# Optimization experiments

Hardware: AMD Instinct MI355X
Metric: run time of the kernel (lower is better)

The kernel has to match this reference:

```python
import jax, jax.numpy as jnp
import numpy as np

F = 128          # feature_size
C = 300          # n_content_dims
V = 100001       # n_nodes + 1 (embedding rows)
N0, N1, N2 = 409600, 40960, 4096   # NodeFlow layer sizes (fanout ~10)
E0, E1 = 409600, 40960             # edges in block0 (L0->L1) and block1 (L1->L2)


def setup_inputs() -> dict:
    key = jax.random.key(0)
    ks = jax.random.split(key, 24)
    std = 1.0 / F
    xav_p = float(np.sqrt(6.0 / (C + F)))   # xavier_uniform for proj Linear(C->F)
    xav_c = float(np.sqrt(6.0 / (2 * F + F)))  # xavier_uniform for conv Linear(2F->F)
    return {
        'nid0': jax.random.randint(ks[0], (N0,), 0, 100000),
        'nid1': jax.random.randint(ks[1], (N1,), 0, 100000),
        'nid2': jax.random.randint(ks[2], (N2,), 0, 100000),
        'content0': jax.random.normal(ks[3], (N0, C), jnp.float32),
        'content1': jax.random.normal(ks[4], (N1, C), jnp.float32),
        'content2': jax.random.normal(ks[5], (N2, C), jnp.float32),
        'block0_src': jax.random.randint(ks[6], (E0,), 0, N0),
        'block0_dst': jax.random.randint(ks[7], (E0,), 0, N1),
        'block1_src': jax.random.randint(ks[8], (E1,), 0, N1),
        'block1_dst': jax.random.randint(ks[9], (E1,), 0, N2),
        'node_emb': jax.random.normal(ks[10], (V, F), jnp.float32) * std,
        'Wp0': jax.random.uniform(ks[11], (F, C), jnp.float32, -xav_p, xav_p),
        'bp0': jnp.zeros((F,), jnp.float32),
        'Wp1': jax.random.uniform(ks[12], (F, C), jnp.float32, -xav_p, xav_p),
        'bp1': jnp.zeros((F,), jnp.float32),
        'Wp2': jax.random.uniform(ks[13], (F, C), jnp.float32, -xav_p, xav_p),
        'bp2': jnp.zeros((F,), jnp.float32),
        'Wc0': jax.random.uniform(ks[14], (F, 2 * F), jnp.float32, -xav_c, xav_c),
        'bc0': jnp.zeros((F,), jnp.float32),
        'Wc1': jax.random.uniform(ks[15], (F, 2 * F), jnp.float32, -xav_c, xav_c),
        'bc1': jnp.zeros((F,), jnp.float32),
    }


def _embed(node_emb, nid, content, Wp, bp):
    # h = node_emb(nid + 1) + LeakyReLU(content @ Wp.T + bp)   (dropout is eval no-op)
    return node_emb[nid + 1] + jax.nn.leaky_relu(content @ Wp.T + bp)


def _conv(h_src, src, dst, h_self, n_dst, W, b):
    # DGL block_compute: copy_src('h')+sum -> h_agg ; copy_src('one')+sum -> w
    msgs = h_src[src]                                    # [E, F] gather
    h_agg = jax.ops.segment_sum(msgs, dst, num_segments=n_dst)
    w = jax.ops.segment_sum(jnp.ones((src.shape[0],), h_src.dtype), dst,
                            num_segments=n_dst)
    h_agg = (h_agg - h_self) / jnp.maximum(w - 1.0, 1.0)[:, None]
    h_new = jax.nn.leaky_relu(jnp.concatenate([h_self, h_agg], axis=1) @ W.T + b)
    nrm = jnp.maximum(jnp.linalg.norm(h_new, axis=1, keepdims=True), 1e-6)
    return h_new / nrm


def reference(nid0, nid1, nid2, content0, content1, content2,
              block0_src, block0_dst, block1_src, block1_dst,
              node_emb, Wp0, bp0, Wp1, bp1, Wp2, bp2,
              Wc0, bc0, Wc1, bc1):
    h0 = _embed(node_emb, nid0, content0, Wp0, bp0)   # [N0, F]
    h1 = _embed(node_emb, nid1, content1, Wp1, bp1)   # [N1, F]
    h2 = _embed(node_emb, nid2, content2, Wp2, bp2)   # [N2, F]
    h1 = _conv(h0, block0_src, block0_dst, h1, N1, Wc0, bc0)
    h2 = _conv(h1, block1_src, block1_dst, h2, N2, Wc1, bc1)
    return h2
```

## Files before the change

kernel.cpp:

```cpp
#include <hip/hip_runtime.h>
#include <hip/hip_bf16.h>
#include <math.h>

#define F 128
#define C 300
#define CKP 320
#define NKT 10
#define K2F 256
#define N0_ 409600
#define N1_ 40960
#define N2_ 4096
#define E0_ 409600
#define E1_ 40960
#define CAP 64
#define LDA 40

typedef unsigned short u16;
typedef unsigned int u32;
typedef __attribute__((ext_vector_type(8))) short short8;
typedef __attribute__((ext_vector_type(8))) unsigned short u16x8;
typedef __attribute__((ext_vector_type(4))) float f32x4;

__device__ __forceinline__ float lrelu(float x) { return x > 0.f ? x : 0.01f * x; }

__device__ __forceinline__ u16 f2bf(float x) {
  __hip_bfloat16 h = __float2bfloat16(x);
  u16 r; __builtin_memcpy(&r, &h, 2); return r;
}
__device__ __forceinline__ float bf2f(u16 v) {
  union { u32 u; float f; } c; c.u = ((u32)v) << 16; return c.f;
}

#define GLOAD_LDS16(gp, lp) \
  __builtin_amdgcn_global_load_lds( \
      (const __attribute__((address_space(1))) void*)(const void*)(gp), \
      (__attribute__((address_space(3))) void*)(lp), 16, 0, 0)

__global__ __launch_bounds__(256) void zero_kernel(float4* __restrict__ p, int n4) {
  int i = blockIdx.x * 256 + threadIdx.x;
  if (i < n4) p[i] = make_float4(0.f, 0.f, 0.f, 0.f);
}

__global__ __launch_bounds__(256) void convert_all(
    const float* __restrict__ Wp0, const float* __restrict__ Wp1,
    const float* __restrict__ Wp2, const float* __restrict__ Wc0,
    const float* __restrict__ Wc1,
    u16* __restrict__ Wpb0, u16* __restrict__ Wpb1, u16* __restrict__ Wpb2,
    u16* __restrict__ Wcb0, u16* __restrict__ Wcb1)
{
  int i = blockIdx.x * 256 + threadIdx.x;
  const int P = F * CKP, Q = F * K2F;
  const float* W; u16* O; int K, KP, j;
  if      (i < P)         { W = Wp0; O = Wpb0; K = C;   KP = CKP; j = i; }
  else if (i < 2 * P)     { W = Wp1; O = Wpb1; K = C;   KP = CKP; j = i - P; }
  else if (i < 3 * P)     { W = Wp2; O = Wpb2; K = C;   KP = CKP; j = i - 2 * P; }
  else if (i < 3 * P + Q) { W = Wc0; O = Wcb0; K = K2F; KP = K2F; j = i - 3 * P; }
  else if (i < 3 * P + 2 * Q) { W = Wc1; O = Wcb1; K = K2F; KP = K2F; j = i - 3 * P - Q; }
  else return;
  int f = j / KP, k = j - f * KP;
  O[j] = (k < K) ? f2bf(W[(size_t)f * K + k]) : (u16)0;
}

__global__ __launch_bounds__(256) void build_csr(
    const int* __restrict__ b0s, const int* __restrict__ b0d,
    const int* __restrict__ b1s, const int* __restrict__ b1d,
    int* __restrict__ deg0, int* __restrict__ deg1,
    int* __restrict__ csr0, int* __restrict__ csr1)
{
  int e = blockIdx.x * 256 + threadIdx.x;
  if (e < E0_) {
    int d = b0d[e];
    int slot = atomicAdd(&deg0[d], 1);
    if (slot < CAP) csr0[(size_t)d * CAP + slot] = b0s[e];
  } else {
    int e1 = e - E0_;
    if (e1 < E1_) {
      int d = b1d[e1];
      int slot = atomicAdd(&deg1[d], 1);
      if (slot < CAP) csr1[(size_t)d * CAP + slot] = b1s[e1];
    }
  }
}

struct Afrag { float4 x00, x01, x10, x11; };

__global__ __launch_bounds__(256, 2) void embed_all(
    const float* __restrict__ content0, const float* __restrict__ content1,
    const float* __restrict__ content2,
    const u16* __restrict__ Wpb0, const u16* __restrict__ Wpb1,
    const u16* __restrict__ Wpb2,
    const float* __restrict__ bp0, const float* __restrict__ bp1,
    const float* __restrict__ bp2,
    const int* __restrict__ nid0, const int* __restrict__ nid1,
    const int* __restrict__ nid2,
    const float* __restrict__ emb,
    u16* __restrict__ out0, u16* __restrict__ out1, u16* __restrict__ out2)
{
  __shared__ u16 Bs[NKT * 128 * 32];
  const int t = threadIdx.x, lane = t & 63, w = t >> 6;
  const int b = blockIdx.x;

  const float* content; const u16* Wpb; const float* bp; const int* nid;
  u16* out; int ostride, row0;
  if (b < N0_ / 128) {
    content = content0; Wpb = Wpb0; bp = bp0; nid = nid0;
    out = out0; ostride = F; row0 = b * 128;
  } else if (b < N0_ / 128 + N1_ / 128) {
    content = content1; Wpb = Wpb1; bp = bp1; nid = nid1;
    out = out1; ostride = 2 * F; row0 = (b - N0_ / 128) * 128;
  } else {
    content = content2; Wpb = Wpb2; bp = bp2; nid = nid2;
    out = out2; ostride = 2 * F; row0 = (b - N0_ / 128 - N1_ / 128) * 128;
  }

  {
    const int j_in = lane >> 2, u_in = lane & 3;
#pragma unroll
    for (int cc = 0; cc < 20; ++cc) {
      int c = w * 20 + cc;
      int kt = c >> 3, j0 = (c & 7) * 16;
      int j = j0 + j_in;
      int u = u_in ^ (j & 3);
      const u16* gp = Wpb + (size_t)j * CKP + kt * 32 + u * 8;
      GLOAD_LDS16(gp, &Bs[(size_t)(kt * 128 + j0) * 32]);
    }
  }

  f32x4 acc[2][8];
#pragma unroll
  for (int fr = 0; fr < 2; ++fr)
#pragma unroll
    for (int fc = 0; fc < 8; ++fc) {
      acc[fr][fc][0] = 0.f; acc[fr][fc][1] = 0.f;
      acc[fr][fc][2] = 0.f; acc[fr][fc][3] = 0.f;
    }

  const int frow = lane & 15, g = lane >> 4;
  const float* c0p = content + (size_t)(row0 + w * 32 + frow) * C;
  const float* c1p = c0p + (size_t)16 * C;

  auto loadA = [&](int kt) -> Afrag {
    Afrag r;
    int col = kt * 32 + g * 8;
    if (kt < NKT - 1) {
      r.x00 = *(const float4*)(c0p + col); r.x01 = *(const float4*)(c0p + col + 4);
      r.x10 = *(const float4*)(c1p + col); r.x11 = *(const float4*)(c1p + col + 4);
    } else {
      float v0[8], v1[8];
#pragma unroll
      for (int i = 0; i < 8; ++i) {
        int cc = col + i;
        v0[i] = (cc < C) ? c0p[cc] : 0.f;
        v1[i] = (cc < C) ? c1p[cc] : 0.f;
      }
      r.x00 = make_float4(v0[0], v0[1], v0[2], v0[3]);
      r.x01 = make_float4(v0[4], v0[5], v0[6], v0[7]);
      r.x10 = make_float4(v1[0], v1[1], v1[2], v1[3]);
      r.x11 = make_float4(v1[4], v1[5], v1[6], v1[7]);
    }
    return r;
  };

  const int bsw = (g ^ (frow & 3)) * 8;
  auto compute = [&](const Afrag& a, int kt) {
    u16x8 a0v, a1v;
    a0v[0]=f2bf(a.x00.x); a0v[1]=f2bf(a.x00.y); a0v[2]=f2bf(a.x00.z); a0v[3]=f2bf(a.x00.w);
    a0v[4]=f2bf(a.x01.x); a0v[5]=f2bf(a.x01.y); a0v[6]=f2bf(a.x01.z); a0v[7]=f2bf(a.x01.w);
    a1v[0]=f2bf(a.x10.x); a1v[1]=f2bf(a.x10.y); a1v[2]=f2bf(a.x10.z); a1v[3]=f2bf(a.x10.w);
    a1v[4]=f2bf(a.x11.x); a1v[5]=f2bf(a.x11.y); a1v[6]=f2bf(a.x11.z); a1v[7]=f2bf(a.x11.w);
    short8 a0 = *(short8*)&a0v, a1 = *(short8*)&a1v;
#pragma unroll
    for (int fc = 0; fc < 8; ++fc) {
      short8 bfr = *(const short8*)&Bs[(size_t)(kt * 128 + fc * 16 + frow) * 32 + bsw];
      acc[0][fc] = __builtin_amdgcn_mfma_f32_16x16x32_bf16(a0, bfr, acc[0][fc], 0, 0, 0);
      acc[1][fc] = __builtin_amdgcn_mfma_f32_16x16x32_bf16(a1, bfr, acc[1][fc], 0, 0, 0);
    }
  };

  Afrag A0 = loadA(0);
  Afrag A1 = loadA(1);
  Afrag A2 = loadA(2);
  __syncthreads();
  Afrag A3 = loadA(3); compute(A0, 0);
  A0 = loadA(4);       compute(A1, 1);
  A1 = loadA(5);       compute(A2, 2);
  A2 = loadA(6);       compute(A3, 3);
  A3 = loadA(7);       compute(A0, 4);
  A0 = loadA(8);       compute(A1, 5);
  A1 = loadA(9);       compute(A2, 6);
  compute(A3, 7);
  compute(A0, 8);
  compute(A1, 9);

  float bpv[8];
#pragma unroll
  for (int fc = 0; fc < 8; ++fc) bpv[fc] = bp[fc * 16 + frow];
#pragma unroll
  for (int fr = 0; fr < 2; ++fr) {
#pragma unroll
    for (int q = 0; q < 4; ++q) {
      int n = row0 + w * 32 + fr * 16 + g * 4 + q;
      int gi = nid[n] + 1;
      const float* erow = emb + (size_t)gi * F;
      u16* orow = out + (size_t)n * ostride;
#pragma unroll
      for (int fc = 0; fc < 8; ++fc) {
        int col = fc * 16 + frow;
        float v = acc[fr][fc][q] + bpv[fc];
        orow[col] = f2bf(erow[col] + lrelu(v));
      }
    }
  }
}

__global__ __launch_bounds__(256) void gather_xa(
    const u16* __restrict__ hsrc, const int* __restrict__ csr,
    const int* __restrict__ deg, u16* __restrict__ xcat)
{
  int d = blockIdx.x * 4 + (threadIdx.x >> 6);
  int lane = threadIdx.x & 63;
  u32 hv = *(const u32*)&xcat[(size_t)d * (2 * F) + lane * 2];
  float h0f = bf2f((u16)(hv & 0xffff)), h1f = bf2f((u16)(hv >> 16));
  int dg = deg[d];
  int n = dg < CAP ? dg : CAP;
  const int* cp = csr + (size_t)d * CAP;
  float s0 = 0.f, s1 = 0.f;
  int j = 0;
  for (; j + 4 <= n; j += 4) {
    int i0 = cp[j], i1 = cp[j + 1], i2 = cp[j + 2], i3 = cp[j + 3];
    u32 v0 = *(const u32*)&hsrc[(size_t)i0 * F + lane * 2];
    u32 v1 = *(const u32*)&hsrc[(size_t)i1 * F + lane * 2];
    u32 v2 = *(const u32*)&hsrc[(size_t)i2 * F + lane * 2];
    u32 v3 = *(const u32*)&hsrc[(size_t)i3 * F + lane * 2];
    s0 += bf2f((u16)(v0 & 0xffff)) + bf2f((u16)(v1 & 0xffff))
        + bf2f((u16)(v2 & 0xffff)) + bf2f((u16)(v3 & 0xffff));
    s1 += bf2f((u16)(v0 >> 16)) + bf2f((u16)(v1 >> 16))
        + bf2f((u16)(v2 >> 16)) + bf2f((u16)(v3 >> 16));
  }
  for (; j < n; ++j) {
    u32 v = *(const u32*)&hsrc[(size_t)cp[j] * F + lane * 2];
    s0 += bf2f((u16)(v & 0xffff));
    s1 += bf2f((u16)(v >> 16));
  }
  float inv = 1.f / fmaxf((float)dg - 1.f, 1.f);
  u16 a0 = f2bf((s0 - h0f) * inv), a1 = f2bf((s1 - h1f) * inv);
  *(u32*)&xcat[(size_t)d * (2 * F) + F + lane * 2] = ((u32)a1 << 16) | a0;
}

template<int F32OUT>
__global__ __launch_bounds__(256) void conv_mfma(
    const u16* __restrict__ xcat, const u16* __restrict__ Wcb,
    const float* __restrict__ bc, u16* __restrict__ outb,
    float* __restrict__ outf)
{
  __shared__ u16 As[128][LDA];
  __shared__ u16 Bs[128][LDA];
  const int t = threadIdx.x;
  const int lane = t & 63, w = t >> 6;
  const int row0 = blockIdx.x * 128;

  f32x4 acc[2][8];
#pragma unroll
  for (int fr = 0; fr < 2; ++fr)
#pragma unroll
    for (int fc = 0; fc < 8; ++fc) {
      acc[fr][fc][0] = 0.f; acc[fr][fc][1] = 0.f;
      acc[fr][fc][2] = 0.f; acc[fr][fc][3] = 0.f;
    }

  for (int k0 = 0; k0 < K2F; k0 += 32) {
    if (k0) __syncthreads();
#pragma unroll
    for (int it = 0; it < 2; ++it) {
      int cc = it * 256 + t;
      int r = cc >> 2, kc = (cc & 3) * 8;
      *(u16x8*)&As[r][kc] = *(const u16x8*)&xcat[(size_t)(row0 + r) * K2F + k0 + kc];
      *(u16x8*)&Bs[r][kc] = *(const u16x8*)&Wcb[(size_t)r * K2F + k0 + kc];
    }
    __syncthreads();

    const int frow = lane & 15;
    const int kc = (lane >> 4) * 8;
    short8 a0 = *(const short8*)&As[w * 32 + frow][kc];
    short8 a1 = *(const short8*)&As[w * 32 + 16 + frow][kc];
#pragma unroll
    for (int fc = 0; fc < 8; ++fc) {
      short8 b = *(const short8*)&Bs[fc * 16 + frow][kc];
      acc[0][fc] = __builtin_amdgcn_mfma_f32_16x16x32_bf16(a0, b, acc[0][fc], 0, 0, 0);
      acc[1][fc] = __builtin_amdgcn_mfma_f32_16x16x32_bf16(a1, b, acc[1][fc], 0, 0, 0);
    }
  }

  float bcv[8];
#pragma unroll
  for (int fc = 0; fc < 8; ++fc) bcv[fc] = bc[fc * 16 + (lane & 15)];
#pragma unroll
  for (int fr = 0; fr < 2; ++fr) {
#pragma unroll
    for (int q = 0; q < 4; ++q) {
      float x[8];
      float ss = 0.f;
#pragma unroll
      for (int fc = 0; fc < 8; ++fc) {
        x[fc] = lrelu(acc[fr][fc][q] + bcv[fc]);
        ss += x[fc] * x[fc];
      }
#pragma unroll
      for (int m = 8; m >= 1; m >>= 1) ss += __shfl_xor(ss, m, 64);
      float nrm = 1.f / fmaxf(sqrtf(ss), 1e-6f);
      int n = row0 + w * 32 + fr * 16 + (lane >> 4) * 4 + q;
#pragma unroll
      for (int fc = 0; fc < 8; ++fc) {
        int col = fc * 16 + (lane & 15);
        if (F32OUT) outf[(size_t)n * F + col] = x[fc] * nrm;
        else        outb[(size_t)n * F + col] = f2bf(x[fc] * nrm);
      }
    }
  }
}

extern "C" void kernel_launch(void* const* d_in, const int* in_sizes, int n_in,
                              void* d_out, int out_size, void* d_ws, size_t ws_size,
                              hipStream_t stream) {
  const int*   nid0     = (const int*)d_in[0];
  const int*   nid1     = (const int*)d_in[1];
  const int*   nid2     = (const int*)d_in[2];
  const float* content0 = (const float*)d_in[3];
  const float* content1 = (const float*)d_in[4];
  const float* content2 = (const float*)d_in[5];
  const int*   b0s      = (const int*)d_in[6];
  const int*   b0d      = (const int*)d_in[7];
  const int*   b1s      = (const int*)d_in[8];
  const int*   b1d      = (const int*)d_in[9];
  const float* emb      = (const float*)d_in[10];
  const float* Wp0      = (const float*)d_in[11];
  const float* bp0      = (const float*)d_in[12];
  const float* Wp1      = (const float*)d_in[13];
  const float* bp1      = (const float*)d_in[14];
  const float* Wp2      = (const float*)d_in[15];
  const float* bp2      = (const float*)d_in[16];
  const float* Wc0      = (const float*)d_in[17];
  const float* bc0      = (const float*)d_in[18];
  const float* Wc1      = (const float*)d_in[19];
  const float* bc1      = (const float*)d_in[20];

  u16* wsu = (u16*)d_ws;
  u16* h0b   = wsu;
  u16* xcat1 = h0b + (size_t)N0_ * F;
  u16* xcat2 = xcat1 + (size_t)N1_ * 2 * F;
  u16* h1nb  = xcat2 + (size_t)N2_ * 2 * F;
  u16* Wpb0  = h1nb + (size_t)N1_ * F;
  u16* Wpb1  = Wpb0 + (size_t)F * CKP;
  u16* Wpb2  = Wpb1 + (size_t)F * CKP;
  u16* Wcb0  = Wpb2 + (size_t)F * CKP;
  u16* Wcb1  = Wcb0 + (size_t)F * K2F;
  int* deg0  = (int*)(Wcb1 + (size_t)F * K2F);
  int* deg1  = deg0 + N1_;
  int* csr0  = deg1 + N2_;
  int* csr1  = csr0 + (size_t)N1_ * CAP;

  const int zn4 = (N1_ + N2_) / 4;
  zero_kernel<<<(zn4 + 255) / 256, 256, 0, stream>>>((float4*)deg0, zn4);

  build_csr<<<(E0_ + E1_ + 255) / 256, 256, 0, stream>>>(
      b0s, b0d, b1s, b1d, deg0, deg1, csr0, csr1);

  convert_all<<<(3 * F * CKP + 2 * F * K2F + 255) / 256, 256, 0, stream>>>(
      Wp0, Wp1, Wp2, Wc0, Wc1, Wpb0, Wpb1, Wpb2, Wcb0, Wcb1);

  embed_all<<<(N0_ + N1_ + N2_) / 128, 256, 0, stream>>>(
      content0, content1, content2, Wpb0, Wpb1, Wpb2,
      bp0, bp1, bp2, nid0, nid1, nid2, emb, h0b, xcat1, xcat2);

  gather_xa<<<N1_ / 4, 256, 0, stream>>>(h0b, csr0, deg0, xcat1);
  conv_mfma<0><<<N1_ / 128, 256, 0, stream>>>(xcat1, Wcb0, bc0, h1nb, nullptr);

  gather_xa<<<N2_ / 4, 256, 0, stream>>>(h1nb, csr1, deg1, xcat2);
  conv_mfma<1><<<N2_ / 128, 256, 0, stream>>>(xcat2, Wcb1, bc1, nullptr, (float*)d_out);
}
```

Before: 318.1 us.

## Drop LDS weight staging in embed kernel; read B from global, halve tile

The embed GEMM no longer stages the bf16 projection weights into shared memory. Each wave now reads its B fragments straight from global memory (the weights are small and should stay cache-resident), which removes the block barrier and the 80KB LDS footprint. Each wave now handles 16 rows instead of 32, so a block covers 64 rows and the grid doubles. Launch bounds rise to 4 blocks per SM for higher occupancy. In exchange, weight reuse per block drops and every MFMA issues a global or L2 load for its B operand, which may add latency.

```diff
diff --git a/kernel.cpp b/kernel.cpp
--- a/kernel.cpp
+++ b/kernel.cpp
@@ -17,6 +17,7 @@
 
 typedef unsigned short u16;
 typedef unsigned int u32;
+typedef __attribute__((ext_vector_type(2))) unsigned int u32x2;
 typedef __attribute__((ext_vector_type(8))) short short8;
 typedef __attribute__((ext_vector_type(8))) unsigned short u16x8;
 typedef __attribute__((ext_vector_type(4))) float f32x4;
@@ -30,11 +31,6 @@
 __device__ __forceinline__ float bf2f(u16 v) {
   union { u32 u; float f; } c; c.u = ((u32)v) << 16; return c.f;
 }
-
-#define GLOAD_LDS16(gp, lp) \
-  __builtin_amdgcn_global_load_lds( \
-      (const __attribute__((address_space(1))) void*)(const void*)(gp), \
-      (__attribute__((address_space(3))) void*)(lp), 16, 0, 0)
 
 __global__ __launch_bounds__(256) void zero_kernel(float4* __restrict__ p, int n4) {
   int i = blockIdx.x * 256 + threadIdx.x;
@@ -82,9 +78,9 @@
   }
 }
 
-struct Afrag { float4 x00, x01, x10, x11; };
-
-__global__ __launch_bounds__(256, 2) void embed_all(
+struct A16 { float4 x0, x1; };
+
+__global__ __launch_bounds__(256, 4) void embed_all(
     const float* __restrict__ content0, const float* __restrict__ content1,
     const float* __restrict__ content2,
     const u16* __restrict__ Wpb0, const u16* __restrict__ Wpb1,
@@ -96,98 +92,74 @@
     const float* __restrict__ emb,
     u16* __restrict__ out0, u16* __restrict__ out1, u16* __restrict__ out2)
 {
-  __shared__ u16 Bs[NKT * 128 * 32];
   const int t = threadIdx.x, lane = t & 63, w = t >> 6;
   const int b = blockIdx.x;
 
   const float* content; const u16* Wpb; const float* bp; const int* nid;
-  u16* out; int ostride, row0;
-  if (b < N0_ / 128) {
+  u16* out; int ostride, rowb;
+  if (b < N0_ / 64) {
     content = content0; Wpb = Wpb0; bp = bp0; nid = nid0;
-    out = out0; ostride = F; row0 = b * 128;
-  } else if (b < N0_ / 128 + N1_ / 128) {
+    out = out0; ostride = F; rowb = b * 64;
+  } else if (b < N0_ / 64 + N1_ / 64) {
     content = content1; Wpb = Wpb1; bp = bp1; nid = nid1;
-    out = out1; ostride = 2 * F; row0 = (b - N0_ / 128) * 128;
+    out = out1; ostride = 2 * F; rowb = (b - N0_ / 64) * 64;
   } else {
     content = content2; Wpb = Wpb2; bp = bp2; nid = nid2;
-    out = out2; ostride = 2 * F; row0 = (b - N0_ / 128 - N1_ / 128) * 128;
-  }
-
-  {
-    const int j_in = lane >> 2, u_in = lane & 3;
-#pragma unroll
-    for (int cc = 0; cc < 20; ++cc) {
-      int c = w * 20 + cc;
-      int kt = c >> 3, j0 = (c & 7) * 16;
-      int j = j0 + j_in;
-      int u = u_in ^ (j & 3);
-      const u16* gp = Wpb + (size_t)j * CKP + kt * 32 + u * 8;
-      GLOAD_LDS16(gp, &Bs[(size_t)(kt * 128 + j0) * 32]);
-    }
-  }
-
-  f32x4 acc[2][8];
-#pragma unroll
-  for (int fr = 0; fr < 2; ++fr)
-#pragma unroll
-    for (int fc = 0; fc < 8; ++fc) {
-      acc[fr][fc][0] = 0.f; acc[fr][fc][1] = 0.f;
-      acc[fr][fc][2] = 0.f; acc[fr][fc][3] = 0.f;
-    }
+    out = out2; ostride = 2 * F; rowb = (b - N0_ / 64 - N1_ / 64) * 64;
+  }
 
   const int frow = lane & 15, g = lane >> 4;
-  const float* c0p = content + (size_t)(row0 + w * 32 + frow) * C;
-  const float* c1p = c0p + (size_t)16 * C;
-
-  auto loadA = [&](int kt) -> Afrag {
-    Afrag r;
+  const int row0 = rowb + w * 16;
+  const float* c0p = content + (size_t)(row0 + frow) * C;
+  const u16* bbase = Wpb + (size_t)frow * CKP + g * 8;
+
+  f32x4 acc[8];
+#pragma unroll
+  for (int fc = 0; fc < 8; ++fc) {
+    acc[fc][0] = 0.f; acc[fc][1] = 0.f; acc[fc][2] = 0.f; acc[fc][3] = 0.f;
+  }
+
+  auto loadA = [&](int kt) -> A16 {
+    A16 r;
     int col = kt * 32 + g * 8;
     if (kt < NKT - 1) {
-      r.x00 = *(const float4*)(c0p + col); r.x01 = *(const float4*)(c0p + col + 4);
-      r.x10 = *(const float4*)(c1p + col); r.x11 = *(const float4*)(c1p + col + 4);
+      r.x0 = *(const float4*)(c0p + col);
+      r.x1 = *(const float4*)(c0p + col + 4);
     } else {
-      float v0[8], v1[8];
+      float v[8];
 #pragma unroll
       for (int i = 0; i < 8; ++i) {
         int cc = col + i;
-        v0[i] = (cc < C) ? c0p[cc] : 0.f;
-        v1[i] = (cc < C) ? c1p[cc] : 0.f;
+        v[i] = (cc < C) ? c0p[cc] : 0.f;
       }
-      r.x00 = make_float4(v0[0], v0[1], v0[2], v0[3]);
-      r.x01 = make_float4(v0[4], v0[5], v0[6], v0[7]);
-      r.x10 = make_float4(v1[0], v1[1], v1[2], v1[3]);
-      r.x11 = make_float4(v1[4], v1[5], v1[6], v1[7]);
+      r.x0 = make_float4(v[0], v[1], v[2], v[3]);
+      r.x1 = make_float4(v[4], v[5], v[6], v[7]);
     }
     return r;
   };
 
-  const int bsw = (g ^ (frow & 3)) * 8;
-  auto compute = [&](const Afrag& a, int kt) {
-    u16x8 a0v, a1v;
-    a0v[0]=f2bf(a.x00.x); a0v[1]=f2bf(a.x00.y); a0v[2]=f2bf(a.x00.z); a0v[3]=f2bf(a.x00.w);
-    a0v[4]=f2bf(a.x01.x); a0v[5]=f2bf(a.x01.y); a0v[6]=f2bf(a.x01.z); a0v[7]=f2bf(a.x01.w);
-    a1v[0]=f2bf(a.x10.x); a1v[1]=f2bf(a.x10.y); a1v[2]=f2bf(a.x10.z); a1v[3]=f2bf(a.x10.w);
-    a1v[4]=f2bf(a.x11.x); a1v[5]=f2bf(a.x11.y); a1v[6]=f2bf(a.x11.z); a1v[7]=f2bf(a.x11.w);
-    short8 a0 = *(short8*)&a0v, a1 = *(short8*)&a1v;
+  auto compute = [&](const A16& a, int kt) {
+    u16x8 av;
+    av[0]=f2bf(a.x0.x); av[1]=f2bf(a.x0.y); av[2]=f2bf(a.x0.z); av[3]=f2bf(a.x0.w);
+    av[4]=f2bf(a.x1.x); av[5]=f2bf(a.x1.y); av[6]=f2bf(a.x1.z); av[7]=f2bf(a.x1.w);
+    short8 a0 = *(short8*)&av;
 #pragma unroll
     for (int fc = 0; fc < 8; ++fc) {
-      short8 bfr = *(const short8*)&Bs[(size_t)(kt * 128 + fc * 16 + frow) * 32 + bsw];
-      acc[0][fc] = __builtin_amdgcn_mfma_f32_16x16x32_bf16(a0, bfr, acc[0][fc], 0, 0, 0);
-      acc[1][fc] = __builtin_amdgcn_mfma_f32_16x16x32_bf16(a1, bfr, acc[1][fc], 0, 0, 0);
+      short8 bfr = *(const short8*)(bbase + (size_t)(fc * 16) * CKP + kt * 32);
+      acc[fc] = __builtin_amdgcn_mfma_f32_16x16x32_bf16(a0, bfr, acc[fc], 0, 0, 0);
     }
   };
 
-  Afrag A0 = loadA(0);
-  Afrag A1 = loadA(1);
-  Afrag A2 = loadA(2);
-  __syncthreads();
-  Afrag A3 = loadA(3); compute(A0, 0);
-  A0 = loadA(4);       compute(A1, 1);
-  A1 = loadA(5);       compute(A2, 2);
-  A2 = loadA(6);       compute(A3, 3);
-  A3 = loadA(7);       compute(A0, 4);
-  A0 = loadA(8);       compute(A1, 5);
-  A1 = loadA(9);       compute(A2, 6);
+  A16 A0 = loadA(0);
+  A16 A1 = loadA(1);
+  A16 A2 = loadA(2);
+  A16 A3 = loadA(3); compute(A0, 0);
+  A0 = loadA(4);     compute(A1, 1);
+  A1 = loadA(5);     compute(A2, 2);
+  A2 = loadA(6);     compute(A3, 3);
+  A3 = loadA(7);     compute(A0, 4);
+  A0 = loadA(8);     compute(A1, 5);
+  A1 = loadA(9);     compute(A2, 6);
   compute(A3, 7);
   compute(A0, 8);
   compute(A1, 9);
@@ -196,19 +168,16 @@
 #pragma unroll
   for (int fc = 0; fc < 8; ++fc) bpv[fc] = bp[fc * 16 + frow];
 #pragma unroll
-  for (int fr = 0; fr < 2; ++fr) {
-#pragma unroll
-    for (int q = 0; q < 4; ++q) {
-      int n = row0 + w * 32 + fr * 16 + g * 4 + q;
-      int gi = nid[n] + 1;
-      const float* erow = emb + (size_t)gi * F;
-      u16* orow = out + (size_t)n * ostride;
-#pragma unroll
-      for (int fc = 0; fc < 8; ++fc) {
-        int col = fc * 16 + frow;
-        float v = acc[fr][fc][q] + bpv[fc];
-        orow[col] = f2bf(erow[col] + lrelu(v));
-      }
+  for (int q = 0; q < 4; ++q) {
+    int n = row0 + g * 4 + q;
+    int gi = nid[n] + 1;
+    const float* erow = emb + (size_t)gi * F;
+    u16* orow = out + (size_t)n * ostride;
+#pragma unroll
+    for (int fc = 0; fc < 8; ++fc) {
+      int col = fc * 16 + frow;
+      float v = acc[fc][q] + bpv[fc];
+      orow[col] = f2bf(erow[col] + lrelu(v));
     }
   }
 }
@@ -368,7 +337,7 @@
   convert_all<<<(3 * F * CKP + 2 * F * K2F + 255) / 256, 256, 0, stream>>>(
       Wp0, Wp1, Wp2, Wc0, Wc1, Wpb0, Wpb1, Wpb2, Wcb0, Wcb1);
 
-  embed_all<<<(N0_ + N1_ + N2_) / 128, 256, 0, stream>>>(
+  embed_all<<<(N0_ + N1_ + N2_) / 64, 256, 0, stream>>>(
       content0, content1, content2, Wpb0, Wpb1, Wpb2,
       bp0, bp1, bp2, nid0, nid1, nid2, emb, h0b, xcat1, xcat2);
 
```

Measured after the change: 528.0 us. 66.0% more time.
